# Kernel tuning notes

Measured on AMD Instinct MI355X. Metric: run time of the kernel, lower is better.

Reference implementation:

```python
import jax, jax.numpy as jnp
import numpy as np

N_API, N_FILE, E = 50000, 20000, 250000
N_INP, N_OUT, H = 512, 256, 3


def setup_inputs() -> dict:
    key = jax.random.key(0)
    ks = jax.random.split(key, 16)
    s = 0.05
    return {
        "emb_api": jax.random.normal(ks[0], (N_API, N_INP), jnp.float32),
        "emb_file": jax.random.normal(ks[1], (N_FILE, N_INP), jnp.float32),
        "e_tensor": jax.random.normal(ks[2], (E,), jnp.float32),
        "src": jax.random.randint(ks[3], (E,), 0, N_API, jnp.int32),
        "dst": jax.random.randint(ks[4], (E,), 0, N_FILE, jnp.int32),
        # api_proj / file_proj (Linear n_inp->n_inp), stored as [in,out]
        "Wapi": jax.random.normal(ks[5], (N_INP, N_INP), jnp.float32) * s,
        "bapi": jnp.zeros((N_INP,), jnp.float32),
        "Wfile": jax.random.normal(ks[6], (N_INP, N_INP), jnp.float32) * s,
        "bfile": jnp.zeros((N_INP,), jnp.float32),
        # GATConv fc_src / fc_dst (no bias), attn vectors, output bias
        "Wsrc": jax.random.normal(ks[7], (N_INP, H * N_OUT), jnp.float32) * s,
        "Wdst": jax.random.normal(ks[8], (N_INP, H * N_OUT), jnp.float32) * s,
        "attn_l": jax.random.normal(ks[9], (H, N_OUT), jnp.float32) * s,
        "attn_r": jax.random.normal(ks[10], (H, N_OUT), jnp.float32) * s,
        "gat_bias": jnp.zeros((H * N_OUT,), jnp.float32),
        # head_linear (3*n_out -> n_out)
        "Whead": jax.random.normal(ks[11], (H * N_OUT, N_OUT), jnp.float32) * s,
        "bhead": jnp.zeros((N_OUT,), jnp.float32),
    }


def reference(emb_api, emb_file, e_tensor, src, dst,
              Wapi, bapi, Wfile, bfile,
              Wsrc, Wdst, attn_l, attn_r, gat_bias,
              Whead, bhead):
    nd = emb_file.shape[0]
    # dual linear projections
    x_api = emb_api @ Wapi + bapi            # [Nsrc, n_inp]
    x_file = emb_file @ Wfile + bfile        # [Ndst, n_inp]
    # GATConv (bipartite, DGL semantics): per-head linear, additive attention
    fsrc = (x_api @ Wsrc).reshape(-1, H, N_OUT)   # [Nsrc, H, D]
    fdst = (x_file @ Wdst).reshape(-1, H, N_OUT)  # [Ndst, H, D]
    el = jnp.sum(fsrc * attn_l, axis=-1)          # [Nsrc, H]
    er = jnp.sum(fdst * attn_r, axis=-1)          # [Ndst, H]
    e = jax.nn.leaky_relu(el[src] + er[dst], 0.2)  # [E, H]
    # edge softmax over incoming edges of each dst node
    m = jax.ops.segment_max(e, dst, num_segments=nd)   # [Ndst, H]
    a = jnp.exp(e - m[dst])
    z = jax.ops.segment_sum(a, dst, num_segments=nd)   # [Ndst, H]
    alpha = a / z[dst]                                  # [E, H]
    # weighted aggregation of source messages
    rst = jax.ops.segment_sum(alpha[:, :, None] * fsrc[src], dst,
                              num_segments=nd)          # [Ndst, H, D]
    rst = rst + gat_bias.reshape(H, N_OUT)
    # head fusion
    z_str = rst.reshape(nd, H * N_OUT) @ Whead + bhead  # [Ndst, n_out]
    return z_str
```

## Files before the change

### kernel.cpp

```cpp
#include <hip/hip_runtime.h>
#include <hip/hip_bf16.h>
#include <cstdint>
#include <cstddef>

#define N_INP 512
#define N_OUT 256
#define H 3
#define HD (H * N_OUT)
#define AGG_D (H * (N_INP + 1))
#define HSTR 522
#define KP 1568

typedef __attribute__((ext_vector_type(8))) short short8;
typedef __attribute__((ext_vector_type(4))) float f32x4;

__device__ inline unsigned short f2bf(float x) {
    union { float f; unsigned u; } v; v.f = x;
    unsigned r = v.u + 0x7fffu + ((v.u >> 16) & 1u);
    return (unsigned short)(r >> 16);
}
__device__ inline float bflo2f(unsigned u) {
    union { unsigned u; float f; } v; v.u = u << 16; return v.f;
}
__device__ inline float bfhi2f(unsigned u) {
    union { unsigned u; float f; } v; v.u = u & 0xffff0000u; return v.f;
}

__device__ inline void glds16(const void* g, void* l) {
    __builtin_amdgcn_global_load_lds(
        (const __attribute__((address_space(1))) void*)g,
        (__attribute__((address_space(3))) void*)l, 16, 0, 0);
}

__global__ void zero_int_kernel(int* p, int n) {
    int i = blockIdx.x * blockDim.x + threadIdx.x;
    if (i < n) p[i] = 0;
}

__global__ void initC_kernel(float* __restrict__ C, const float* __restrict__ bz, int n) {
    int i = blockIdx.x * blockDim.x + threadIdx.x;
    if (i < n) C[i] = bz[i & (N_OUT - 1)];
}

__global__ __launch_bounds__(256) void v_kernel(
    const float* __restrict__ Wsrc, const float* __restrict__ Wdst,
    const float* __restrict__ attn_l, const float* __restrict__ attn_r,
    float* __restrict__ v) {
    int wave = threadIdx.x >> 6, lane = threadIdx.x & 63;
    int idx = blockIdx.x * 4 + wave;
    if (idx >= 2 * H * N_INP) return;
    int which = idx / (H * N_INP);
    int r = idx % (H * N_INP);
    int h = r / N_INP, o = r % N_INP;
    const float* W = which ? Wdst : Wsrc;
    const float* at = which ? attn_r : attn_l;
    float s = 0.f;
#pragma unroll
    for (int i = 0; i < N_OUT / 64; ++i) {
        int t = lane + i * 64;
        s += W[(size_t)o * HD + h * N_OUT + t] * at[h * N_OUT + t];
    }
#pragma unroll
    for (int off = 32; off >= 1; off >>= 1) s += __shfl_xor(s, off, 64);
    if (lane == 0) v[idx] = s;
}

__global__ __launch_bounds__(256) void u_kernel(
    const float* __restrict__ Wapi, const float* __restrict__ Wfile,
    const float* __restrict__ bapi, const float* __restrict__ bfile,
    const float* __restrict__ v, float* __restrict__ u,
    float* __restrict__ ebias) {
    int wave = threadIdx.x >> 6, lane = threadIdx.x & 63;
    int idx = blockIdx.x * 4 + wave;
    if (idx < 2 * H * N_INP) {
        int which = idx / (H * N_INP);
        int r = idx % (H * N_INP);
        int h = r / N_INP, i = r % N_INP;
        const float* W = which ? Wfile : Wapi;
        const float* vv = v + which * (H * N_INP) + h * N_INP;
        float s = 0.f;
#pragma unroll
        for (int j = 0; j < N_INP / 64; ++j) {
            int o = lane + j * 64;
            s += W[(size_t)i * N_INP + o] * vv[o];
        }
#pragma unroll
        for (int off = 32; off >= 1; off >>= 1) s += __shfl_xor(s, off, 64);
        if (lane == 0) u[idx] = s;
    } else if (idx < 2 * H * N_INP + 6) {
        int k = idx - 2 * H * N_INP;
        int which = k / H, h = k % H;
        const float* b = which ? bfile : bapi;
        const float* vv = v + which * (H * N_INP) + h * N_INP;
        float s = 0.f;
#pragma unroll
        for (int j = 0; j < N_INP / 64; ++j) {
            int o = lane + j * 64;
            s += b[o] * vv[o];
        }
#pragma unroll
        for (int off = 32; off >= 1; off >>= 1) s += __shfl_xor(s, off, 64);
        if (lane == 0) ebias[k] = s;
    }
}

__global__ __launch_bounds__(256) void elr_kernel(
    const float* __restrict__ emb, const float* __restrict__ u,
    const float* __restrict__ ebias, float* __restrict__ out,
    unsigned short* __restrict__ embB, int n) {
    __shared__ float su[H * N_INP];
    for (int i = threadIdx.x; i < H * N_INP; i += 256) su[i] = u[i];
    __syncthreads();
    int wave = threadIdx.x >> 6;
    int lane = threadIdx.x & 63;
    int node = blockIdx.x * 4 + wave;
    if (node >= n) return;
    const float4* row = (const float4*)(emb + (size_t)node * N_INP);
    float4 v0 = row[lane];
    float4 v1 = row[64 + lane];
    int c0 = lane * 4, c1 = 256 + lane * 4;
    if (embB) {
        unsigned short* o = embB + (size_t)node * N_INP;
        ushort4 p0, p1;
        p0.x = f2bf(v0.x); p0.y = f2bf(v0.y); p0.z = f2bf(v0.z); p0.w = f2bf(v0.w);
        p1.x = f2bf(v1.x); p1.y = f2bf(v1.y); p1.z = f2bf(v1.z); p1.w = f2bf(v1.w);
        *(ushort4*)(o + c0) = p0;
        *(ushort4*)(o + c1) = p1;
    }
    float d[H];
#pragma unroll
    for (int h = 0; h < H; ++h) {
        const float* uh = su + h * N_INP;
        d[h] = v0.x * uh[c0] + v0.y * uh[c0 + 1] + v0.z * uh[c0 + 2] + v0.w * uh[c0 + 3]
             + v1.x * uh[c1] + v1.y * uh[c1 + 1] + v1.z * uh[c1 + 2] + v1.w * uh[c1 + 3];
#pragma unroll
        for (int off = 32; off >= 1; off >>= 1) d[h] += __shfl_xor(d[h], off, 64);
    }
    if (lane == 0) {
#pragma unroll
        for (int h = 0; h < H; ++h) out[(size_t)node * H + h] = d[h] + ebias[h];
    }
}

__global__ void count_kernel(const int* __restrict__ dst, int* __restrict__ counts, int E) {
    int e = blockIdx.x * blockDim.x + threadIdx.x;
    if (e < E) atomicAdd(&counts[dst[e]], 1);
}

__global__ __launch_bounds__(1024) void scan_kernel(const int* __restrict__ counts,
                                                    int* __restrict__ offsets,
                                                    int* __restrict__ cursor, int n) {
    __shared__ int part[1024];
    int t = threadIdx.x;
    const int CH = (n + 1023) / 1024;
    int lo = t * CH, hi = min(lo + CH, n);
    int s = 0;
    for (int i = lo; i < hi; ++i) s += counts[i];
    part[t] = s;
    __syncthreads();
    for (int off = 1; off < 1024; off <<= 1) {
        int v = (t >= off) ? part[t - off] : 0;
        __syncthreads();
        part[t] += v;
        __syncthreads();
    }
    int base = (t == 0) ? 0 : part[t - 1];
    for (int i = lo; i < hi; ++i) {
        offsets[i] = base; cursor[i] = base;
        base += counts[i];
    }
    if (t == 1023) offsets[n] = part[1023];
}

__global__ void scatter_kernel(const int* __restrict__ src, const int* __restrict__ dst,
                               int* __restrict__ cursor, int* __restrict__ csr_src, int E) {
    int e = blockIdx.x * blockDim.x + threadIdx.x;
    if (e < E) {
        int slot = atomicAdd(&cursor[dst[e]], 1);
        csr_src[slot] = src[e];
    }
}

__global__ __launch_bounds__(256) void alpha_kernel(
    const int* __restrict__ offsets, const int* __restrict__ csr_src,
    const float* __restrict__ el, const float* __restrict__ er,
    float* __restrict__ alpha, int nd) {
    int wave = threadIdx.x >> 6;
    int lane = threadIdx.x & 63;
    int d = blockIdx.x * 4 + wave;
    if (d >= nd) return;
    int lo = offsets[d], hi = offsets[d + 1];
    if (lo == hi) return;
    float er0 = er[(size_t)d * H + 0], er1 = er[(size_t)d * H + 1], er2 = er[(size_t)d * H + 2];
    float m0 = -3.4e38f, m1 = -3.4e38f, m2 = -3.4e38f;
    for (int s = lo + lane; s < hi; s += 64) {
        int u = csr_src[s];
        float e0 = el[(size_t)u * H + 0] + er0; e0 = e0 >= 0.f ? e0 : 0.2f * e0;
        float e1 = el[(size_t)u * H + 1] + er1; e1 = e1 >= 0.f ? e1 : 0.2f * e1;
        float e2 = el[(size_t)u * H + 2] + er2; e2 = e2 >= 0.f ? e2 : 0.2f * e2;
        m0 = fmaxf(m0, e0); m1 = fmaxf(m1, e1); m2 = fmaxf(m2, e2);
    }
#pragma unroll
    for (int off = 32; off >= 1; off >>= 1) {
        m0 = fmaxf(m0, __shfl_xor(m0, off, 64));
        m1 = fmaxf(m1, __shfl_xor(m1, off, 64));
        m2 = fmaxf(m2, __shfl_xor(m2, off, 64));
    }
    float s0 = 0.f, s1 = 0.f, s2 = 0.f;
    for (int s = lo + lane; s < hi; s += 64) {
        int u = csr_src[s];
        float e0 = el[(size_t)u * H + 0] + er0; e0 = e0 >= 0.f ? e0 : 0.2f * e0;
        float e1 = el[(size_t)u * H + 1] + er1; e1 = e1 >= 0.f ? e1 : 0.2f * e1;
        float e2 = el[(size_t)u * H + 2] + er2; e2 = e2 >= 0.f ? e2 : 0.2f * e2;
        float a0 = expf(e0 - m0), a1 = expf(e1 - m1), a2 = expf(e2 - m2);
        alpha[(size_t)s * H + 0] = a0; alpha[(size_t)s * H + 1] = a1; alpha[(size_t)s * H + 2] = a2;
        s0 += a0; s1 += a1; s2 += a2;
    }
#pragma unroll
    for (int off = 32; off >= 1; off >>= 1) {
        s0 += __shfl_xor(s0, off, 64);
        s1 += __shfl_xor(s1, off, 64);
        s2 += __shfl_xor(s2, off, 64);
    }
    float i0 = 1.f / s0, i1 = 1.f / s1, i2 = 1.f / s2;
    for (int s = lo + lane; s < hi; s += 64) {
        alpha[(size_t)s * H + 0] *= i0;
        alpha[(size_t)s * H + 1] *= i1;
        alpha[(size_t)s * H + 2] *= i2;
    }
}

__global__ __launch_bounds__(256) void agg_kernel(
    const int* __restrict__ offsets, const int* __restrict__ csr_src,
    const float* __restrict__ alpha, const unsigned short* __restrict__ embB,
    unsigned short* __restrict__ aggB, int nd) {
    int d = blockIdx.x;
    if (d >= nd) return;
    int tid = threadIdx.x;
    int lo = offsets[d], hi = offsets[d + 1];
    int c = tid * 2;
    float a00 = 0.f, a01 = 0.f, a10 = 0.f, a11 = 0.f, a20 = 0.f, a21 = 0.f;
    for (int s = lo; s < hi; ++s) {
        int u = csr_src[s];
        float w0 = alpha[(size_t)s * H + 0];
        float w1 = alpha[(size_t)s * H + 1];
        float w2 = alpha[(size_t)s * H + 2];
        unsigned v = *(const unsigned*)(embB + (size_t)u * N_INP + c);
        float x = bflo2f(v), y = bfhi2f(v);
        a00 += w0 * x; a01 += w0 * y;
        a10 += w1 * x; a11 += w1 * y;
        a20 += w2 * x; a21 += w2 * y;
    }
    size_t base = (size_t)d * KP;
    *(unsigned*)(aggB + base + 0 * HSTR + c) = (unsigned)f2bf(a00) | ((unsigned)f2bf(a01) << 16);
    *(unsigned*)(aggB + base + 1 * HSTR + c) = (unsigned)f2bf(a10) | ((unsigned)f2bf(a11) << 16);
    *(unsigned*)(aggB + base + 2 * HSTR + c) = (unsigned)f2bf(a20) | ((unsigned)f2bf(a21) << 16);
    if (tid == 0) {
        unsigned short flag = (hi > lo) ? (unsigned short)0x3f80 : (unsigned short)0;
#pragma unroll
        for (int h = 0; h < H; ++h) {
            aggB[base + h * HSTR + 512] = flag;
            for (int z = 513; z < HSTR; ++z) aggB[base + h * HSTR + z] = 0;
        }
        aggB[base + 3 * HSTR + 0] = 0;
        aggB[base + 3 * HSTR + 1] = 0;
    }
}

template <int K>
__global__ __launch_bounds__(256) void wgemm(
    const float* __restrict__ A, int lda, size_t sAz,
    const float* __restrict__ B, int ldb, size_t sBz,
    float* __restrict__ C, int ldc, size_t sCz, int M) {
    A += blockIdx.z * sAz; B += blockIdx.z * sBz; C += blockIdx.z * sCz;
    __shared__ float sA[8 * K];
    __shared__ float red[8 * 256];
    int tid = threadIdx.x;
    int r0 = blockIdx.x * 8;
    int bn = blockIdx.y * 64;
    for (int i = tid; i < 8 * K; i += 256) {
        int r = i / K, k = i % K;
        sA[i] = A[(size_t)(r0 + r) * lda + k];
    }
    __syncthreads();
    int cl = tid & 63, ks = tid >> 6;
    int col = bn + cl;
    const int KC = K / 4;
    float acc[8] = {};
    for (int k0 = ks * KC; k0 < ks * KC + KC; k0 += 8) {
        float b[8];
#pragma unroll
        for (int j = 0; j < 8; ++j) b[j] = B[(size_t)(k0 + j) * ldb + col];
#pragma unroll
        for (int j = 0; j < 8; ++j) {
            float bb = b[j];
#pragma unroll
            for (int i = 0; i < 8; ++i) acc[i] += sA[i * K + k0 + j] * bb;
        }
    }
#pragma unroll
    for (int i = 0; i < 8; ++i) red[i * 256 + ks * 64 + cl] = acc[i];
    __syncthreads();
    for (int t = tid; t < 512; t += 256) {
        int i = t >> 6, c = t & 63;
        float s = red[i * 256 + c] + red[i * 256 + 64 + c]
                + red[i * 256 + 128 + c] + red[i * 256 + 192 + c];
        if (r0 + i < M) C[(size_t)(r0 + i) * ldc + bn + c] = s;
    }
}

__global__ __launch_bounds__(256) void brow_kernel(
    const float* __restrict__ bapi, const float* __restrict__ T,
    const float* __restrict__ gat_bias, const float* __restrict__ Whead,
    const float* __restrict__ bhead,
    float* __restrict__ Mmat, float* __restrict__ bz) {
    int wave = threadIdx.x >> 6, lane = threadIdx.x & 63;
    int idx = blockIdx.x * 4 + wave;
    if (idx < H * N_OUT) {
        int h = idx / N_OUT, j = idx % N_OUT;
        float s = 0.f;
#pragma unroll
        for (int i = 0; i < N_INP / 64; ++i) {
            int cc = lane + i * 64;
            s += bapi[cc] * T[((size_t)h * N_INP + cc) * N_OUT + j];
        }
#pragma unroll
        for (int off = 32; off >= 1; off >>= 1) s += __shfl_xor(s, off, 64);
        if (lane == 0) Mmat[((size_t)(h * 513 + 512)) * N_OUT + j] = s;
    } else if (idx < H * N_OUT + N_OUT) {
        int j = idx - H * N_OUT;
        float s = 0.f;
#pragma unroll
        for (int i = 0; i < HD / 64; ++i) {
            int f = lane + i * 64;
            s += gat_bias[f] * Whead[(size_t)f * N_OUT + j];
        }
#pragma unroll
        for (int off = 32; off >= 1; off >>= 1) s += __shfl_xor(s, off, 64);
        if (lane == 0) bz[j] = s + bhead[j];
    }
}

__global__ void convT_kernel(const float* __restrict__ Mmat, unsigned short* __restrict__ MmatT) {
    int idx = blockIdx.x * blockDim.x + threadIdx.x;
    if (idx >= N_OUT * KP) return;
    int n = idx / KP, k = idx % KP;
    float v = 0.f;
    if (k < H * HSTR) {
        int h = k / HSTR, c = k % HSTR;
        if (c < 513) v = Mmat[((size_t)(h * 513 + c)) * N_OUT + n];
    }
    MmatT[(size_t)n * KP + k] = f2bf(v);
}

__global__ __launch_bounds__(256, 4) void gemm_mfma(
    const unsigned short* __restrict__ A, const unsigned short* __restrict__ BT,
    float* __restrict__ C, int M) {
    __shared__ __align__(16) short As[2][128 * 32];
    __shared__ __align__(16) short Bs[2][128 * 32];
    int tid = threadIdx.x;
    int wave = tid >> 6, lane = tid & 63;
    int bm = blockIdx.y * 128, bn = blockIdx.x * 128;
    int wm = (wave >> 1) * 64, wn = (wave & 1) * 64;
    int quad = lane >> 4, m16 = lane & 15;
    int kz = blockIdx.z;
    int kbeg = kz * 416;
    int kend = (kz == 3) ? KP : kbeg + 416;

    int srow = lane >> 2;
    int schunk = (lane & 3) * 8;

    f32x4 acc[4][4] = {};

    auto stage = [&](int buf, int k0) {
#pragma unroll
        for (int p = 0; p < 2; ++p) {
            int row = p * 64 + wave * 16 + srow;
            int ar = bm + row; if (ar >= M) ar = M - 1;
            glds16(A + (size_t)ar * KP + k0 + schunk, &As[buf][(p * 64 + wave * 16) * 32]);
            glds16(BT + (size_t)(bn + row) * KP + k0 + schunk, &Bs[buf][(p * 64 + wave * 16) * 32]);
        }
    };

    stage(0, kbeg);
    int cur = 0;
    for (int k0 = kbeg; k0 < kend; k0 += 32) {
        if (k0 + 32 < kend) {
            stage(cur ^ 1, k0 + 32);
            asm volatile("s_waitcnt vmcnt(4)" ::: "memory");
        } else {
            asm volatile("s_waitcnt vmcnt(0)" ::: "memory");
        }
        asm volatile("" ::: "memory");
        __builtin_amdgcn_s_barrier();
        asm volatile("" ::: "memory");
        short8 af[4], bf[4];
#pragma unroll
        for (int t = 0; t < 4; ++t) {
            af[t] = *(const short8*)(&As[cur][(wm + t * 16 + m16) * 32 + quad * 8]);
            bf[t] = *(const short8*)(&Bs[cur][(wn + t * 16 + m16) * 32 + quad * 8]);
        }
#pragma unroll
        for (int mt = 0; mt < 4; ++mt)
#pragma unroll
            for (int nt = 0; nt < 4; ++nt)
                acc[mt][nt] = __builtin_amdgcn_mfma_f32_16x16x32_bf16(
                    af[mt], bf[nt], acc[mt][nt], 0, 0, 0);
        asm volatile("" ::: "memory");
        __builtin_amdgcn_s_barrier();
        asm volatile("" ::: "memory");
        cur ^= 1;
    }
#pragma unroll
    for (int mt = 0; mt < 4; ++mt) {
#pragma unroll
        for (int i = 0; i < 4; ++i) {
            int r = bm + wm + mt * 16 + quad * 4 + i;
            if (r >= M) continue;
#pragma unroll
            for (int nt = 0; nt < 4; ++nt) {
                int col = bn + wn + nt * 16 + m16;
                atomicAdd(&C[(size_t)r * N_OUT + col], acc[mt][nt][i]);
            }
        }
    }
}

extern "C" void kernel_launch(void* const* d_in, const int* in_sizes, int n_in,
                              void* d_out, int out_size, void* d_ws, size_t ws_size,
                              hipStream_t stream) {
    const float* emb_api  = (const float*)d_in[0];
    const float* emb_file = (const float*)d_in[1];
    const int*   src      = (const int*)d_in[3];
    const int*   dst      = (const int*)d_in[4];
    const float* Wapi     = (const float*)d_in[5];
    const float* bapi     = (const float*)d_in[6];
    const float* Wfile    = (const float*)d_in[7];
    const float* bfile    = (const float*)d_in[8];
    const float* Wsrc     = (const float*)d_in[9];
    const float* Wdst     = (const float*)d_in[10];
    const float* attn_l   = (const float*)d_in[11];
    const float* attn_r   = (const float*)d_in[12];
    const float* gat_bias = (const float*)d_in[13];
    const float* Whead    = (const float*)d_in[14];
    const float* bhead    = (const float*)d_in[15];
    float* out = (float*)d_out;

    const int NAPI = in_sizes[0] / N_INP;
    const int NFIL = in_sizes[1] / N_INP;
    const int E    = in_sizes[3];

    char* p = (char*)d_ws;
    auto alloc = [&](size_t bytes) -> void* {
        void* r = (void*)p;
        p += (bytes + 255) & ~(size_t)255;
        return r;
    };
    float* el      = (float*)alloc((size_t)NAPI * H * 4);
    float* er      = (float*)alloc((size_t)NFIL * H * 4);
    float* vbuf    = (float*)alloc(2 * H * N_INP * 4);
    float* ubuf    = (float*)alloc(2 * H * N_INP * 4);
    float* ebias   = (float*)alloc(8 * 4);
    float* T       = (float*)alloc((size_t)H * N_INP * N_OUT * 4);
    float* Mmat    = (float*)alloc((size_t)AGG_D * N_OUT * 4);
    float* bz      = (float*)alloc(N_OUT * 4);
    int*   counts  = (int*)alloc((size_t)NFIL * 4);
    int*   offsets = (int*)alloc((size_t)(NFIL + 1) * 4);
    int*   cursor  = (int*)alloc((size_t)NFIL * 4);
    int*   csr_src = (int*)alloc((size_t)E * 4);
    float* alphaB  = (float*)alloc((size_t)E * H * 4);
    unsigned short* embB  = (unsigned short*)alloc((size_t)NAPI * N_INP * 2);
    unsigned short* aggB  = (unsigned short*)alloc((size_t)NFIL * KP * 2);
    unsigned short* MmatT = (unsigned short*)alloc((size_t)N_OUT * KP * 2);
    (void)ws_size; (void)n_in; (void)out_size;

    v_kernel<<<(2 * H * N_INP + 3) / 4, 256, 0, stream>>>(Wsrc, Wdst, attn_l, attn_r, vbuf);
    u_kernel<<<(2 * H * N_INP + 6 + 3) / 4, 256, 0, stream>>>(Wapi, Wfile, bapi, bfile, vbuf, ubuf, ebias);
    wgemm<N_OUT><<<dim3(N_INP / 8, 4, H), 256, 0, stream>>>(
        Wsrc, HD, (size_t)N_OUT,
        Whead, N_OUT, (size_t)N_OUT * N_OUT,
        T, N_OUT, (size_t)N_INP * N_OUT, N_INP);
    wgemm<N_INP><<<dim3(N_INP / 8, 4, H), 256, 0, stream>>>(
        Wapi, N_INP, (size_t)0,
        T, N_OUT, (size_t)N_INP * N_OUT,
        Mmat, N_OUT, (size_t)513 * N_OUT, N_INP);
    brow_kernel<<<(H * N_OUT + N_OUT + 3) / 4, 256, 0, stream>>>(
        bapi, T, gat_bias, Whead, bhead, Mmat, bz);
    convT_kernel<<<(N_OUT * KP + 255) / 256, 256, 0, stream>>>(Mmat, MmatT);
    initC_kernel<<<((size_t)NFIL * N_OUT + 255) / 256, 256, 0, stream>>>(out, bz, NFIL * N_OUT);

    elr_kernel<<<(NAPI + 3) / 4, 256, 0, stream>>>(emb_api, ubuf, ebias, el, embB, NAPI);
    elr_kernel<<<(NFIL + 3) / 4, 256, 0, stream>>>(emb_file, ubuf + H * N_INP, ebias + 3, er, nullptr, NFIL);

    zero_int_kernel<<<(NFIL + 255) / 256, 256, 0, stream>>>(counts, NFIL);
    count_kernel<<<(E + 255) / 256, 256, 0, stream>>>(dst, counts, E);
    scan_kernel<<<1, 1024, 0, stream>>>(counts, offsets, cursor, NFIL);
    scatter_kernel<<<(E + 255) / 256, 256, 0, stream>>>(src, dst, cursor, csr_src, E);

    alpha_kernel<<<(NFIL + 3) / 4, 256, 0, stream>>>(offsets, csr_src, el, er, alphaB, NFIL);
    agg_kernel<<<NFIL, 256, 0, stream>>>(offsets, csr_src, alphaB, embB, aggB, NFIL);

    gemm_mfma<<<dim3(256 / 128, (NFIL + 127) / 128, 4), 256, 0, stream>>>(
        aggB, MmatT, out, NFIL);
}
```

Baseline: 490.7 us.

## Fuse softmax into aggregation, merge elr launches, drop split-K atomics in GEMM

Merges the two elr launches and the counts zeroing into one kernel. Folds the edge-softmax alpha computation into the aggregation kernel, which stages per-edge weights in shared memory, so the alpha buffer is never written or read. Removes split-K from the final MFMA GEMM: it now writes the output directly with the bias added, instead of an init kernel followed by atomic adds. The trade-off is fewer GEMM blocks (less parallelism) and recomputation of edge scores three times inside aggregation.

```diff
diff --git a/kernel.cpp b/kernel.cpp
--- a/kernel.cpp
+++ b/kernel.cpp
@@ -10,6 +10,7 @@
 #define AGG_D (H * (N_INP + 1))
 #define HSTR 522
 #define KP 1568
+#define GEMM_NT (KP / 32)
 
 typedef __attribute__((ext_vector_type(8))) short short8;
 typedef __attribute__((ext_vector_type(4))) float f32x4;
@@ -32,15 +33,6 @@
         (__attribute__((address_space(3))) void*)l, 16, 0, 0);
 }
 
-__global__ void zero_int_kernel(int* p, int n) {
-    int i = blockIdx.x * blockDim.x + threadIdx.x;
-    if (i < n) p[i] = 0;
-}
-
-__global__ void initC_kernel(float* __restrict__ C, const float* __restrict__ bz, int n) {
-    int i = blockIdx.x * blockDim.x + threadIdx.x;
-    if (i < n) C[i] = bz[i & (N_OUT - 1)];
-}
 
 __global__ __launch_bounds__(256) void v_kernel(
     const float* __restrict__ Wsrc, const float* __restrict__ Wdst,
@@ -104,33 +96,44 @@
     }
 }
 
-__global__ __launch_bounds__(256) void elr_kernel(
-    const float* __restrict__ emb, const float* __restrict__ u,
-    const float* __restrict__ ebias, float* __restrict__ out,
-    unsigned short* __restrict__ embB, int n) {
-    __shared__ float su[H * N_INP];
-    for (int i = threadIdx.x; i < H * N_INP; i += 256) su[i] = u[i];
+__global__ __launch_bounds__(256) void elr2_kernel(
+    const float* __restrict__ embA, const float* __restrict__ embF,
+    const float* __restrict__ u, const float* __restrict__ ebias,
+    float* __restrict__ el, float* __restrict__ er,
+    unsigned short* __restrict__ embB, int* __restrict__ counts,
+    int nA, int nF) {
+    __shared__ float su[2 * H * N_INP];
+    {
+        int zi = blockIdx.x * 256 + threadIdx.x;
+        if (zi < nF) counts[zi] = 0;
+    }
+    for (int i = threadIdx.x; i < 2 * H * N_INP; i += 256) su[i] = u[i];
     __syncthreads();
     int wave = threadIdx.x >> 6;
     int lane = threadIdx.x & 63;
     int node = blockIdx.x * 4 + wave;
-    if (node >= n) return;
-    const float4* row = (const float4*)(emb + (size_t)node * N_INP);
+    if (node >= nA + nF) return;
+    int side = (node >= nA);
+    int nn = side ? node - nA : node;
+    const float* emb = side ? embF : embA;
+    float* out = side ? (er + (size_t)nn * H) : (el + (size_t)nn * H);
+    const float4* row = (const float4*)(emb + (size_t)nn * N_INP);
     float4 v0 = row[lane];
     float4 v1 = row[64 + lane];
     int c0 = lane * 4, c1 = 256 + lane * 4;
-    if (embB) {
-        unsigned short* o = embB + (size_t)node * N_INP;
+    if (!side) {
+        unsigned short* o = embB + (size_t)nn * N_INP;
         ushort4 p0, p1;
         p0.x = f2bf(v0.x); p0.y = f2bf(v0.y); p0.z = f2bf(v0.z); p0.w = f2bf(v0.w);
         p1.x = f2bf(v1.x); p1.y = f2bf(v1.y); p1.z = f2bf(v1.z); p1.w = f2bf(v1.w);
         *(ushort4*)(o + c0) = p0;
         *(ushort4*)(o + c1) = p1;
     }
+    const float* ub = su + side * (H * N_INP);
     float d[H];
 #pragma unroll
     for (int h = 0; h < H; ++h) {
-        const float* uh = su + h * N_INP;
+        const float* uh = ub + h * N_INP;
         d[h] = v0.x * uh[c0] + v0.y * uh[c0 + 1] + v0.z * uh[c0 + 2] + v0.w * uh[c0 + 3]
              + v1.x * uh[c1] + v1.y * uh[c1 + 1] + v1.z * uh[c1 + 2] + v1.w * uh[c1 + 3];
 #pragma unroll
@@ -138,7 +141,7 @@
     }
     if (lane == 0) {
 #pragma unroll
-        for (int h = 0; h < H; ++h) out[(size_t)node * H + h] = d[h] + ebias[h];
+        for (int h = 0; h < H; ++h) out[h] = d[h] + ebias[side * 3 + h];
     }
 }
 
@@ -181,82 +184,116 @@
     }
 }
 
-__global__ __launch_bounds__(256) void alpha_kernel(
+#define AGG_CH 512
+__global__ __launch_bounds__(256) void agg_kernel(
     const int* __restrict__ offsets, const int* __restrict__ csr_src,
     const float* __restrict__ el, const float* __restrict__ er,
-    float* __restrict__ alpha, int nd) {
-    int wave = threadIdx.x >> 6;
-    int lane = threadIdx.x & 63;
-    int d = blockIdx.x * 4 + wave;
-    if (d >= nd) return;
-    int lo = offsets[d], hi = offsets[d + 1];
-    if (lo == hi) return;
-    float er0 = er[(size_t)d * H + 0], er1 = er[(size_t)d * H + 1], er2 = er[(size_t)d * H + 2];
-    float m0 = -3.4e38f, m1 = -3.4e38f, m2 = -3.4e38f;
-    for (int s = lo + lane; s < hi; s += 64) {
-        int u = csr_src[s];
-        float e0 = el[(size_t)u * H + 0] + er0; e0 = e0 >= 0.f ? e0 : 0.2f * e0;
-        float e1 = el[(size_t)u * H + 1] + er1; e1 = e1 >= 0.f ? e1 : 0.2f * e1;
-        float e2 = el[(size_t)u * H + 2] + er2; e2 = e2 >= 0.f ? e2 : 0.2f * e2;
-        m0 = fmaxf(m0, e0); m1 = fmaxf(m1, e1); m2 = fmaxf(m2, e2);
-    }
-#pragma unroll
-    for (int off = 32; off >= 1; off >>= 1) {
-        m0 = fmaxf(m0, __shfl_xor(m0, off, 64));
-        m1 = fmaxf(m1, __shfl_xor(m1, off, 64));
-        m2 = fmaxf(m2, __shfl_xor(m2, off, 64));
-    }
-    float s0 = 0.f, s1 = 0.f, s2 = 0.f;
-    for (int s = lo + lane; s < hi; s += 64) {
-        int u = csr_src[s];
-        float e0 = el[(size_t)u * H + 0] + er0; e0 = e0 >= 0.f ? e0 : 0.2f * e0;
-        float e1 = el[(size_t)u * H + 1] + er1; e1 = e1 >= 0.f ? e1 : 0.2f * e1;
-        float e2 = el[(size_t)u * H + 2] + er2; e2 = e2 >= 0.f ? e2 : 0.2f * e2;
-        float a0 = expf(e0 - m0), a1 = expf(e1 - m1), a2 = expf(e2 - m2);
-        alpha[(size_t)s * H + 0] = a0; alpha[(size_t)s * H + 1] = a1; alpha[(size_t)s * H + 2] = a2;
-        s0 += a0; s1 += a1; s2 += a2;
-    }
-#pragma unroll
-    for (int off = 32; off >= 1; off >>= 1) {
-        s0 += __shfl_xor(s0, off, 64);
-        s1 += __shfl_xor(s1, off, 64);
-        s2 += __shfl_xor(s2, off, 64);
-    }
-    float i0 = 1.f / s0, i1 = 1.f / s1, i2 = 1.f / s2;
-    for (int s = lo + lane; s < hi; s += 64) {
-        alpha[(size_t)s * H + 0] *= i0;
-        alpha[(size_t)s * H + 1] *= i1;
-        alpha[(size_t)s * H + 2] *= i2;
-    }
-}
-
-__global__ __launch_bounds__(256) void agg_kernel(
-    const int* __restrict__ offsets, const int* __restrict__ csr_src,
-    const float* __restrict__ alpha, const unsigned short* __restrict__ embB,
+    const unsigned short* __restrict__ embB,
     unsigned short* __restrict__ aggB, int nd) {
+    __shared__ int su[AGG_CH];
+    __shared__ float sw0[AGG_CH], sw1[AGG_CH], sw2[AGG_CH];
+    __shared__ float sred[12], sm[3], sz[3];
     int d = blockIdx.x;
     if (d >= nd) return;
-    int tid = threadIdx.x;
-    int lo = offsets[d], hi = offsets[d + 1];
+    int tid = threadIdx.x, wave = tid >> 6, lane = tid & 63;
+    int lo = offsets[d], hi = offsets[d + 1], cnt = hi - lo;
+    float er0 = er[(size_t)d * H + 0], er1 = er[(size_t)d * H + 1], er2 = er[(size_t)d * H + 2];
+    float p0 = -3.4e38f, p1 = -3.4e38f, p2 = -3.4e38f;
+    for (int i = tid; i < cnt; i += 256) {
+        int uu = csr_src[lo + i];
+        float e0 = el[(size_t)uu * H + 0] + er0; e0 = e0 >= 0.f ? e0 : 0.2f * e0;
+        float e1 = el[(size_t)uu * H + 1] + er1; e1 = e1 >= 0.f ? e1 : 0.2f * e1;
+        float e2 = el[(size_t)uu * H + 2] + er2; e2 = e2 >= 0.f ? e2 : 0.2f * e2;
+        p0 = fmaxf(p0, e0); p1 = fmaxf(p1, e1); p2 = fmaxf(p2, e2);
+    }
+#pragma unroll
+    for (int off = 32; off >= 1; off >>= 1) {
+        p0 = fmaxf(p0, __shfl_xor(p0, off, 64));
+        p1 = fmaxf(p1, __shfl_xor(p1, off, 64));
+        p2 = fmaxf(p2, __shfl_xor(p2, off, 64));
+    }
+    if (lane == 0) { sred[wave * 3 + 0] = p0; sred[wave * 3 + 1] = p1; sred[wave * 3 + 2] = p2; }
+    __syncthreads();
+    if (tid < 3) {
+        float v = sred[tid];
+        v = fmaxf(v, sred[3 + tid]); v = fmaxf(v, sred[6 + tid]); v = fmaxf(v, sred[9 + tid]);
+        sm[tid] = v;
+    }
+    __syncthreads();
+    float m0 = sm[0], m1 = sm[1], m2 = sm[2];
+    p0 = 0.f; p1 = 0.f; p2 = 0.f;
+    for (int i = tid; i < cnt; i += 256) {
+        int uu = csr_src[lo + i];
+        float e0 = el[(size_t)uu * H + 0] + er0; e0 = e0 >= 0.f ? e0 : 0.2f * e0;
+        float e1 = el[(size_t)uu * H + 1] + er1; e1 = e1 >= 0.f ? e1 : 0.2f * e1;
+        float e2 = el[(size_t)uu * H + 2] + er2; e2 = e2 >= 0.f ? e2 : 0.2f * e2;
+        p0 += expf(e0 - m0); p1 += expf(e1 - m1); p2 += expf(e2 - m2);
+    }
+#pragma unroll
+    for (int off = 32; off >= 1; off >>= 1) {
+        p0 += __shfl_xor(p0, off, 64);
+        p1 += __shfl_xor(p1, off, 64);
+        p2 += __shfl_xor(p2, off, 64);
+    }
+    if (lane == 0) { sred[wave * 3 + 0] = p0; sred[wave * 3 + 1] = p1; sred[wave * 3 + 2] = p2; }
+    __syncthreads();
+    if (tid < 3) sz[tid] = sred[tid] + sred[3 + tid] + sred[6 + tid] + sred[9 + tid];
+    __syncthreads();
+    float iz0 = 1.f / sz[0], iz1 = 1.f / sz[1], iz2 = 1.f / sz[2];
+    const unsigned* ebdw = (const unsigned*)embB;
+    float a00 = 0.f, a01 = 0.f, a10 = 0.f, a11 = 0.f, a20 = 0.f, a21 = 0.f;
+    for (int baseE = lo; baseE < hi; baseE += AGG_CH) {
+        int cc = min(hi - baseE, AGG_CH);
+        for (int i = tid; i < cc; i += 256) {
+            int uu = csr_src[baseE + i];
+            su[i] = uu;
+            float e0 = el[(size_t)uu * H + 0] + er0; e0 = e0 >= 0.f ? e0 : 0.2f * e0;
+            float e1 = el[(size_t)uu * H + 1] + er1; e1 = e1 >= 0.f ? e1 : 0.2f * e1;
+            float e2 = el[(size_t)uu * H + 2] + er2; e2 = e2 >= 0.f ? e2 : 0.2f * e2;
+            sw0[i] = expf(e0 - m0) * iz0;
+            sw1[i] = expf(e1 - m1) * iz1;
+            sw2[i] = expf(e2 - m2) * iz2;
+        }
+        __syncthreads();
+        int i = 0;
+        for (; i + 4 <= cc; i += 4) {
+            int u0 = su[i], u1 = su[i + 1], u2 = su[i + 2], u3 = su[i + 3];
+            unsigned v0 = ebdw[((size_t)u0 << 8) + tid];
+            unsigned v1 = ebdw[((size_t)u1 << 8) + tid];
+            unsigned v2 = ebdw[((size_t)u2 << 8) + tid];
+            unsigned v3 = ebdw[((size_t)u3 << 8) + tid];
+            float w00 = sw0[i], w01 = sw1[i], w02 = sw2[i];
+            float w10 = sw0[i+1], w11 = sw1[i+1], w12 = sw2[i+1];
+            float w20 = sw0[i+2], w21 = sw1[i+2], w22 = sw2[i+2];
+            float w30 = sw0[i+3], w31 = sw1[i+3], w32 = sw2[i+3];
+            float x, y;
+            x = bflo2f(v0); y = bfhi2f(v0);
+            a00 += w00 * x; a01 += w00 * y; a10 += w01 * x; a11 += w01 * y; a20 += w02 * x; a21 += w02 * y;
+            x = bflo2f(v1); y = bfhi2f(v1);
+            a00 += w10 * x; a01 += w10 * y; a10 += w11 * x; a11 += w11 * y; a20 += w12 * x; a21 += w12 * y;
+            x = bflo2f(v2); y = bfhi2f(v2);
+            a00 += w20 * x; a01 += w20 * y; a10 += w21 * x; a11 += w21 * y; a20 += w22 * x; a21 += w22 * y;
+            x = bflo2f(v3); y = bfhi2f(v3);
+            a00 += w30 * x; a01 += w30 * y; a10 += w31 * x; a11 += w31 * y; a20 += w32 * x; a21 += w32 * y;
+        }
+        for (; i < cc; ++i) {
+            int uu = su[i];
+            unsigned v = ebdw[((size_t)uu << 8) + tid];
+            float w0 = sw0[i], w1 = sw1[i], w2 = sw2[i];
+            float x = bflo2f(v), y = bfhi2f(v);
+            a00 += w0 * x; a01 += w0 * y;
+            a10 += w1 * x; a11 += w1 * y;
+            a20 += w2 * x; a21 += w2 * y;
+        }
+        __syncthreads();
+    }
     int c = tid * 2;
-    float a00 = 0.f, a01 = 0.f, a10 = 0.f, a11 = 0.f, a20 = 0.f, a21 = 0.f;
-    for (int s = lo; s < hi; ++s) {
-        int u = csr_src[s];
-        float w0 = alpha[(size_t)s * H + 0];
-        float w1 = alpha[(size_t)s * H + 1];
-        float w2 = alpha[(size_t)s * H + 2];
-        unsigned v = *(const unsigned*)(embB + (size_t)u * N_INP + c);
-        float x = bflo2f(v), y = bfhi2f(v);
-        a00 += w0 * x; a01 += w0 * y;
-        a10 += w1 * x; a11 += w1 * y;
-        a20 += w2 * x; a21 += w2 * y;
-    }
     size_t base = (size_t)d * KP;
     *(unsigned*)(aggB + base + 0 * HSTR + c) = (unsigned)f2bf(a00) | ((unsigned)f2bf(a01) << 16);
     *(unsigned*)(aggB + base + 1 * HSTR + c) = (unsigned)f2bf(a10) | ((unsigned)f2bf(a11) << 16);
     *(unsigned*)(aggB + base + 2 * HSTR + c) = (unsigned)f2bf(a20) | ((unsigned)f2bf(a21) << 16);
     if (tid == 0) {
-        unsigned short flag = (hi > lo) ? (unsigned short)0x3f80 : (unsigned short)0;
+        unsigned short flag = (cnt > 0) ? (unsigned short)0x3f80 : (unsigned short)0;
 #pragma unroll
         for (int h = 0; h < H; ++h) {
             aggB[base + h * HSTR + 512] = flag;
@@ -353,9 +390,9 @@
     MmatT[(size_t)n * KP + k] = f2bf(v);
 }
 
-__global__ __launch_bounds__(256, 4) void gemm_mfma(
+__global__ __launch_bounds__(256) void gemm_mfma(
     const unsigned short* __restrict__ A, const unsigned short* __restrict__ BT,
-    float* __restrict__ C, int M) {
+    const float* __restrict__ bias, float* __restrict__ C, int M) {
     __shared__ __align__(16) short As[2][128 * 32];
     __shared__ __align__(16) short Bs[2][128 * 32];
     int tid = threadIdx.x;
@@ -363,10 +400,6 @@
     int bm = blockIdx.y * 128, bn = blockIdx.x * 128;
     int wm = (wave >> 1) * 64, wn = (wave & 1) * 64;
     int quad = lane >> 4, m16 = lane & 15;
-    int kz = blockIdx.z;
-    int kbeg = kz * 416;
-    int kend = (kz == 3) ? KP : kbeg + 416;
-
     int srow = lane >> 2;
     int schunk = (lane & 3) * 8;
 
@@ -382,31 +415,29 @@
         }
     };
 
-    stage(0, kbeg);
+    stage(0, 0);
+    asm volatile("s_waitcnt vmcnt(0)" ::: "memory");
+    __builtin_amdgcn_s_barrier();
+    asm volatile("" ::: "memory");
     int cur = 0;
-    for (int k0 = kbeg; k0 < kend; k0 += 32) {
-        if (k0 + 32 < kend) {
-            stage(cur ^ 1, k0 + 32);
-            asm volatile("s_waitcnt vmcnt(4)" ::: "memory");
-        } else {
-            asm volatile("s_waitcnt vmcnt(0)" ::: "memory");
-        }
-        asm volatile("" ::: "memory");
-        __builtin_amdgcn_s_barrier();
-        asm volatile("" ::: "memory");
+    for (int t = 0; t < GEMM_NT; ++t) {
+        if (t + 1 < GEMM_NT) stage(cur ^ 1, (t + 1) * 32);
         short8 af[4], bf[4];
 #pragma unroll
-        for (int t = 0; t < 4; ++t) {
-            af[t] = *(const short8*)(&As[cur][(wm + t * 16 + m16) * 32 + quad * 8]);
-            bf[t] = *(const short8*)(&Bs[cur][(wn + t * 16 + m16) * 32 + quad * 8]);
-        }
+        for (int x = 0; x < 4; ++x) {
+            af[x] = *(const short8*)(&As[cur][(wm + x * 16 + m16) * 32 + quad * 8]);
+            bf[x] = *(const short8*)(&Bs[cur][(wn + x * 16 + m16) * 32 + quad * 8]);
+        }
+        asm volatile("s_waitcnt lgkmcnt(0)" ::: "memory");
+        __builtin_amdgcn_sched_barrier(0);
 #pragma unroll
         for (int mt = 0; mt < 4; ++mt)
 #pragma unroll
             for (int nt = 0; nt < 4; ++nt)
                 acc[mt][nt] = __builtin_amdgcn_mfma_f32_16x16x32_bf16(
                     af[mt], bf[nt], acc[mt][nt], 0, 0, 0);
-        asm volatile("" ::: "memory");
+        __builtin_amdgcn_sched_barrier(0);
+        if (t + 1 < GEMM_NT) asm volatile("s_waitcnt vmcnt(0)" ::: "memory");
         __builtin_amdgcn_s_barrier();
         asm volatile("" ::: "memory");
         cur ^= 1;
@@ -420,7 +451,7 @@
 #pragma unroll
             for (int nt = 0; nt < 4; ++nt) {
                 int col = bn + wn + nt * 16 + m16;
-                atomicAdd(&C[(size_t)r * N_OUT + col], acc[mt][nt][i]);
+                C[(size_t)r * N_OUT + col] = acc[mt][nt][i] + bias[col];
             }
         }
     }
@@ -468,7 +499,6 @@
     int*   offsets = (int*)alloc((size_t)(NFIL + 1) * 4);
     int*   cursor  = (int*)alloc((size_t)NFIL * 4);
     int*   csr_src = (int*)alloc((size_t)E * 4);
-    float* alphaB  = (float*)alloc((size_t)E * H * 4);
     unsigned short* embB  = (unsigned short*)alloc((size_t)NAPI * N_INP * 2);
     unsigned short* aggB  = (unsigned short*)alloc((size_t)NFIL * KP * 2);
     unsigned short* MmatT = (unsigned short*)alloc((size_t)N_OUT * KP * 2);
@@ -487,19 +517,16 @@
     brow_kernel<<<(H * N_OUT + N_OUT + 3) / 4, 256, 0, stream>>>(
         bapi, T, gat_bias, Whead, bhead, Mmat, bz);
     convT_kernel<<<(N_OUT * KP + 255) / 256, 256, 0, stream>>>(Mmat, MmatT);
-    initC_kernel<<<((size_t)NFIL * N_OUT + 255) / 256, 256, 0, stream>>>(out, bz, NFIL * N_OUT);
-
-    elr_kernel<<<(NAPI + 3) / 4, 256, 0, stream>>>(emb_api, ubuf, ebias, el, embB, NAPI);
-    elr_kernel<<<(NFIL + 3) / 4, 256, 0, stream>>>(emb_file, ubuf + H * N_INP, ebias + 3, er, nullptr, NFIL);
-
-    zero_int_kernel<<<(NFIL + 255) / 256, 256, 0, stream>>>(counts, NFIL);
+
+    elr2_kernel<<<(NAPI + NFIL + 3) / 4, 256, 0, stream>>>(
+        emb_api, emb_file, ubuf, ebias, el, er, embB, counts, NAPI, NFIL);
+
     count_kernel<<<(E + 255) / 256, 256, 0, stream>>>(dst, counts, E);
     scan_kernel<<<1, 1024, 0, stream>>>(counts, offsets, cursor, NFIL);
     scatter_kernel<<<(E + 255) / 256, 256, 0, stream>>>(src, dst, cursor, csr_src, E);
 
-    alpha_kernel<<<(NFIL + 3) / 4, 256, 0, stream>>>(offsets, csr_src, el, er, alphaB, NFIL);
-    agg_kernel<<<NFIL, 256, 0, stream>>>(offsets, csr_src, alphaB, embB, aggB, NFIL);
-
-    gemm_mfma<<<dim3(256 / 128, (NFIL + 127) / 128, 4), 256, 0, stream>>>(
-        aggB, MmatT, out, NFIL);
-}
+    agg_kernel<<<NFIL, 256, 0, stream>>>(offsets, csr_src, el, er, embB, aggB, NFIL);
+
+    gemm_mfma<<<dim3(2, (NFIL + 127) / 128), 256, 0, stream>>>(
+        aggB, MmatT, bz, out, NFIL);
+}
```

After: 455.9 us. 1.08x faster.
